# Performance work log

Measured on AMD Instinct MI355X. Metric: run time of the kernel, lower is better.

## Reference

```python
import jax, jax.numpy as jnp
import numpy as np

SEQ_LEN, BATCH, HID, INP = 512, 256, 256, 256


def setup_inputs() -> dict:
    key = jax.random.key(0)
    ks = jax.random.split(key, 6)
    s = 1.0 / np.sqrt(HID)  # torch GRUCell init scale
    return {
        "carry": jnp.zeros((BATCH, HID), jnp.float32),
        "seq_inputs": jax.random.normal(ks[0], (SEQ_LEN, BATCH, INP), jnp.float32),
        "seq_resets": jax.random.randint(ks[1], (SEQ_LEN, BATCH), 0, 2, jnp.int32),
        "w_ih": jax.random.uniform(ks[2], (3 * HID, INP), jnp.float32, -s, s),
        "w_hh": jax.random.uniform(ks[3], (3 * HID, HID), jnp.float32, -s, s),
        "b_ih": jax.random.uniform(ks[4], (3 * HID,), jnp.float32, -s, s),
        "b_hh": jax.random.uniform(ks[5], (3 * HID,), jnp.float32, -s, s),
    }


def reference(carry, seq_inputs, seq_resets, w_ih, w_hh, b_ih, b_hh):
    # Precompute the input-side projection for all timesteps in one GEMM.
    gi_all = jnp.einsum('tbi,gi->tbg', seq_inputs, w_ih) + b_ih  # (T,B,3H)

    def step(h, xs):
        gi, reset_t = xs
        h = jnp.where(reset_t[:, None] > 0, jnp.zeros_like(h), h)
        gh = h @ w_hh.T + b_hh  # (B,3H)
        i_r, i_z, i_n = jnp.split(gi, 3, axis=1)
        h_r, h_z, h_n = jnp.split(gh, 3, axis=1)
        r = jax.nn.sigmoid(i_r + h_r)
        z = jax.nn.sigmoid(i_z + h_z)
        n = jnp.tanh(i_n + r * h_n)
        h_new = (1.0 - z) * n + z * h
        return h_new, h_new

    h_final, outputs = jax.lax.scan(step, carry, (gi_all, seq_resets))
    return h_final, outputs
```

## Files before the change

### kernel.cpp

```cpp
#include <hip/hip_runtime.h>
#include <hip/hip_bf16.h>
#include <hip/hip_fp16.h>


#define T_LEN 512
#define BATCH 256
#define HID   256
#define G3    768

typedef __attribute__((ext_vector_type(8))) short s16x8;
typedef __attribute__((ext_vector_type(4))) float fx4;

#define MFMA16 __builtin_amdgcn_mfma_f32_16x16x32_bf16

__device__ __forceinline__ unsigned short f2bf(float f) {
  union { float f; unsigned u; } v; v.f = f;
  unsigned r = v.u + 0x7fffu + ((v.u >> 16) & 1u);
  return (unsigned short)(r >> 16);
}

__device__ __forceinline__ s16x8 pack8(float4 a, float4 b) {
  s16x8 f;
  f[0] = (short)f2bf(a.x); f[1] = (short)f2bf(a.y);
  f[2] = (short)f2bf(a.z); f[3] = (short)f2bf(a.w);
  f[4] = (short)f2bf(b.x); f[5] = (short)f2bf(b.y);
  f[6] = (short)f2bf(b.z); f[7] = (short)f2bf(b.w);
  return f;
}

__device__ __forceinline__ void load_weights(const float* __restrict__ W,
                                             s16x8 (&wr)[2][8], char* Wlds,
                                             int tid, int wid, int col, int kgrp) {
#pragma unroll
  for (int n = 0; n < 2; ++n) {
    int g = n * 256 + wid * 16 + col;
#pragma unroll
    for (int s8 = 0; s8 < 8; ++s8) {
      int k = s8 * 32 + kgrp * 8;
      const float4* p = (const float4*)(W + g * 256 + k);
      wr[n][s8] = pack8(p[0], p[1]);
    }
  }
#pragma unroll
  for (int q = 0; q < 8; ++q) {
    int li = tid + q * 1024;
    int wv = li >> 9, s8 = (li >> 6) & 7, l = li & 63;
    int g = 512 + wv * 16 + (l & 15);
    int k = s8 * 32 + (l >> 4) * 8;
    const float4* p = (const float4*)(W + g * 256 + k);
    *(s16x8*)(Wlds + li * 16) = pack8(p[0], p[1]);
  }
}

__global__ __launch_bounds__(1024) void gi_proj_kernel(
    const float* __restrict__ X, const float* __restrict__ w_ih,
    const float* __restrict__ b_ih, const float* __restrict__ b_hh,
    __half* __restrict__ gi) {
  __shared__ __align__(16) char Wlds[131072];
  __shared__ __align__(16) char Ald[8192];

  const int tid = threadIdx.x;
  const int wid = tid >> 6, lane = tid & 63;
  const int col = lane & 15, kgrp = lane >> 4;

  s16x8 wr[2][8];
  load_weights(w_ih, wr, Wlds, tid, wid, col, kgrp);

  float bias0, bias1, bias2;
  {
    int gb = wid * 16 + col;
    bias0 = b_ih[gb]       + b_hh[gb];
    bias1 = b_ih[256 + gb] + b_hh[256 + gb];
    bias2 = b_ih[512 + gb];
  }

  const int e4 = tid * 4;
  const int srow = e4 >> 8, sk = e4 & 255;
  const unsigned sbyte = ((unsigned)(srow * 512 + sk * 2)) ^ ((unsigned)(srow & 7) << 4);

  float4 xcur = *(const float4*)(X + (size_t)(blockIdx.x * 16 + srow) * 256 + sk);

  for (int chunk = blockIdx.x; chunk < (T_LEN * BATCH) / 16; chunk += 256) {
    __syncthreads();
    {
      unsigned lo = (unsigned)f2bf(xcur.x) | ((unsigned)f2bf(xcur.y) << 16);
      unsigned hi = (unsigned)f2bf(xcur.z) | ((unsigned)f2bf(xcur.w) << 16);
      uint2 v; v.x = lo; v.y = hi;
      *(uint2*)(Ald + sbyte) = v;
    }
    int nchunk = chunk + 256;
    if (nchunk < (T_LEN * BATCH) / 16)
      xcur = *(const float4*)(X + (size_t)(nchunk * 16 + srow) * 256 + sk);
    __syncthreads();

    fx4 acc0 = {0.f, 0.f, 0.f, 0.f}, acc1 = acc0, acc2 = acc0;
#pragma unroll
    for (int s8 = 0; s8 < 8; ++s8) {
      unsigned aoff = ((unsigned)(col * 512 + (s8 * 32 + kgrp * 8) * 2)) ^
                      ((unsigned)(col & 7) << 4);
      s16x8 af = *(const s16x8*)(Ald + aoff);
      s16x8 w2 = *(const s16x8*)(Wlds + ((wid * 8 + s8) * 64 + lane) * 16);
      acc0 = MFMA16(af, wr[0][s8], acc0, 0, 0, 0);
      acc1 = MFMA16(af, wr[1][s8], acc1, 0, 0, 0);
      acc2 = MFMA16(af, w2, acc2, 0, 0, 0);
    }

    size_t m0 = (size_t)chunk * 16;
#pragma unroll
    for (int j = 0; j < 4; ++j) {
      size_t m = m0 + kgrp * 4 + j;
      __half* gp = gi + m * G3 + wid * 16 + col;
      gp[0]   = __float2half(acc0[j] + bias0);
      gp[256] = __float2half(acc1[j] + bias1);
      gp[512] = __float2half(acc2[j] + bias2);
    }
  }
}

__global__ __launch_bounds__(1024) void gru_scan_kernel(
    const float* __restrict__ carry, const __half* __restrict__ gi,
    const int* __restrict__ resets, const float* __restrict__ w_hh,
    const float* __restrict__ b_hh, float* __restrict__ out) {
  __shared__ __align__(16) char Wlds[131072];
  __shared__ __align__(16) char Ald[8192];
  __shared__ int lastreset[16];

  const int tid = threadIdx.x;
  const int wid = tid >> 6, lane = tid & 63;
  const int col = lane & 15, kgrp = lane >> 4;
  const int c = blockIdx.x >> 4, bt = blockIdx.x & 15;
  const int b0 = bt * 16, t0 = c * 32, t1 = t0 + 32;
  const int hid = wid * 16 + col;

  s16x8 wr[2][8];
  load_weights(w_hh, wr, Wlds, tid, wid, col, kgrp);
  const float bhhn = b_hh[512 + hid];

  int s, useCarry;
  if (c == 0) {
    s = 0; useCarry = 1;
  } else {
    if (tid < 16) lastreset[tid] = -1;
    for (int base = t0 - 64;; base -= 64) {
      __syncthreads();
      int tt = base + (tid >> 4);
      if (tt >= 0 && tt < t0) {
        if (resets[tt * BATCH + b0 + (tid & 15)] != 0)
          atomicMax(&lastreset[tid & 15], tt);
      }
      __syncthreads();
      int mn = t0, all = 1;
#pragma unroll
      for (int i = 0; i < 16; ++i) {
        int v = lastreset[i];
        all &= (v >= 0) ? 1 : 0;
        mn = min(mn, v < 0 ? t0 : v);
      }
      if (all) { s = mn; useCarry = 0; break; }
      if (base <= 0) { s = 0; useCarry = 1; break; }
    }
  }

  {
    int e4 = tid * 4, row = e4 >> 8, k = e4 & 255;
    int rst = resets[s * BATCH + b0 + row];
    float4 v = {0.f, 0.f, 0.f, 0.f};
    if (useCarry && !rst) v = *(const float4*)(carry + (size_t)(b0 + row) * HID + k);
    unsigned lo = (unsigned)f2bf(v.x) | ((unsigned)f2bf(v.y) << 16);
    unsigned hi = (unsigned)f2bf(v.z) | ((unsigned)f2bf(v.w) << 16);
    unsigned byteoff = ((unsigned)(row * 512 + k * 2)) ^ ((unsigned)(row & 7) << 4);
    uint2 u; u.x = lo; u.y = hi;
    *(uint2*)(Ald + byteoff) = u;
  }
  float hprev[4];
#pragma unroll
  for (int j = 0; j < 4; ++j) {
    int b = kgrp * 4 + j;
    int rst = resets[s * BATCH + b0 + b];
    float hv = 0.f;
    if (useCarry && !rst) hv = carry[(size_t)(b0 + b) * HID + hid];
    hprev[j] = hv;
  }
  __syncthreads();

  for (int t = s; t < t1; ++t) {
    __half gr[4], gz[4], gn[4];
#pragma unroll
    for (int j = 0; j < 4; ++j) {
      const __half* gp = gi + ((size_t)t * BATCH + b0 + kgrp * 4 + j) * G3 + hid;
      gr[j] = gp[0]; gz[j] = gp[256]; gn[j] = gp[512];
    }
    int4 rn = {0, 0, 0, 0};
    if (t + 1 < T_LEN) rn = *(const int4*)(resets + (t + 1) * BATCH + b0 + kgrp * 4);

    fx4 acc0 = {0.f, 0.f, 0.f, 0.f}, acc1 = acc0, acc2 = acc0;
#pragma unroll
    for (int s8 = 0; s8 < 8; ++s8) {
      unsigned aoff = ((unsigned)(col * 512 + (s8 * 32 + kgrp * 8) * 2)) ^
                      ((unsigned)(col & 7) << 4);
      s16x8 af = *(const s16x8*)(Ald + aoff);
      s16x8 w2 = *(const s16x8*)(Wlds + ((wid * 8 + s8) * 64 + lane) * 16);
      acc0 = MFMA16(af, wr[0][s8], acc0, 0, 0, 0);
      acc1 = MFMA16(af, wr[1][s8], acc1, 0, 0, 0);
      acc2 = MFMA16(af, w2, acc2, 0, 0, 0);
    }
    __syncthreads();

    const bool wr_out = (t >= t0);
    float* op = out + 65536 + ((size_t)t * BATCH + b0) * HID;
#pragma unroll
    for (int j = 0; j < 4; ++j) {
      int b = kgrp * 4 + j;
      float pr = __half2float(gr[j]) + acc0[j];
      float pz = __half2float(gz[j]) + acc1[j];
      float r = __builtin_amdgcn_rcpf(1.f + __expf(-pr));
      float z = __builtin_amdgcn_rcpf(1.f + __expf(-pz));
      float pn = __half2float(gn[j]) + r * (acc2[j] + bhhn);
      float n = 1.f - 2.f * __builtin_amdgcn_rcpf(1.f + __expf(2.f * pn));
      float hnew = (1.f - z) * n + z * hprev[j];
      if (wr_out) op[(size_t)b * HID + hid] = hnew;
      int rj = (j == 0) ? rn.x : (j == 1) ? rn.y : (j == 2) ? rn.z : rn.w;
      float hk = rj ? 0.f : hnew;
      hprev[j] = hk;
      unsigned hoff = ((unsigned)(b * 512 + hid * 2)) ^ ((unsigned)(b & 7) << 4);
      *(unsigned short*)(Ald + hoff) = f2bf(hk);
    }
    __syncthreads();
  }

  if (c == 15) {
#pragma unroll
    for (int j = 0; j < 4; ++j)
      out[(size_t)(b0 + kgrp * 4 + j) * HID + hid] = hprev[j];
  }
}

extern "C" void kernel_launch(void* const* d_in, const int* in_sizes, int n_in,
                              void* d_out, int out_size, void* d_ws, size_t ws_size,
                              hipStream_t stream) {
  const float* carry = (const float*)d_in[0];
  const float* X     = (const float*)d_in[1];
  const int*   rsts  = (const int*)d_in[2];
  const float* w_ih  = (const float*)d_in[3];
  const float* w_hh  = (const float*)d_in[4];
  const float* b_ih  = (const float*)d_in[5];
  const float* b_hh  = (const float*)d_in[6];
  float* out = (float*)d_out;

  const size_t gi_bytes = (size_t)T_LEN * BATCH * G3 * sizeof(__half);
  if (ws_size < gi_bytes) return;
  __half* gi = (__half*)d_ws;

  gi_proj_kernel<<<256, 1024, 0, stream>>>(X, w_ih, b_ih, b_hh, gi);
  gru_scan_kernel<<<256, 1024, 0, stream>>>(carry, gi, rsts, w_hh, b_hh, out);
}
```

Before: 303.5 us.

## Double-buffer hidden state, prefetch gate inputs, transpose gi layout for vector loads

The hidden-state LDS tile is double-buffered so each timestep needs one barrier instead of two, and the barrier becomes a lighter custom s_barrier. The gi intermediate is stored gate-major and hidden-major with batch innermost, so each lane reads and writes four contiguous halves as one vector instead of scalar gathers. Next-step gate inputs and resets are prefetched a step ahead, and scan block IDs are remapped across batch tiles. This adds LDS and register pressure and relies on manual waitcnt and scheduling correctness.

```diff
diff --git a/kernel.cpp b/kernel.cpp
--- a/kernel.cpp
+++ b/kernel.cpp
@@ -6,12 +6,14 @@
 #define T_LEN 512
 #define BATCH 256
 #define HID   256
-#define G3    768
 
 typedef __attribute__((ext_vector_type(8))) short s16x8;
 typedef __attribute__((ext_vector_type(4))) float fx4;
+typedef __attribute__((ext_vector_type(4))) unsigned short u16x4;
 
 #define MFMA16 __builtin_amdgcn_mfma_f32_16x16x32_bf16
+#define GATE_STRIDE 65536u
+#define T_STRIDE    196608u
 
 __device__ __forceinline__ unsigned short f2bf(float f) {
   union { float f; unsigned u; } v; v.f = f;
@@ -52,12 +54,19 @@
   }
 }
 
+__device__ __forceinline__ void soft_barrier() {
+  asm volatile("s_waitcnt lgkmcnt(0)" ::: "memory");
+  __builtin_amdgcn_s_barrier();
+  __builtin_amdgcn_sched_barrier(0);
+  asm volatile("" ::: "memory");
+}
+
 __global__ __launch_bounds__(1024) void gi_proj_kernel(
     const float* __restrict__ X, const float* __restrict__ w_ih,
     const float* __restrict__ b_ih, const float* __restrict__ b_hh,
     __half* __restrict__ gi) {
   __shared__ __align__(16) char Wlds[131072];
-  __shared__ __align__(16) char Ald[8192];
+  __shared__ __align__(16) char Ald[2][8192];
 
   const int tid = threadIdx.x;
   const int wid = tid >> 6, lane = tid & 63;
@@ -80,40 +89,46 @@
 
   float4 xcur = *(const float4*)(X + (size_t)(blockIdx.x * 16 + srow) * 256 + sk);
 
+  int parity = 0;
   for (int chunk = blockIdx.x; chunk < (T_LEN * BATCH) / 16; chunk += 256) {
-    __syncthreads();
+    char* ab = Ald[parity];
     {
       unsigned lo = (unsigned)f2bf(xcur.x) | ((unsigned)f2bf(xcur.y) << 16);
       unsigned hi = (unsigned)f2bf(xcur.z) | ((unsigned)f2bf(xcur.w) << 16);
       uint2 v; v.x = lo; v.y = hi;
-      *(uint2*)(Ald + sbyte) = v;
+      *(uint2*)(ab + sbyte) = v;
     }
     int nchunk = chunk + 256;
     if (nchunk < (T_LEN * BATCH) / 16)
       xcur = *(const float4*)(X + (size_t)(nchunk * 16 + srow) * 256 + sk);
-    __syncthreads();
+
+    soft_barrier();
 
     fx4 acc0 = {0.f, 0.f, 0.f, 0.f}, acc1 = acc0, acc2 = acc0;
 #pragma unroll
     for (int s8 = 0; s8 < 8; ++s8) {
       unsigned aoff = ((unsigned)(col * 512 + (s8 * 32 + kgrp * 8) * 2)) ^
                       ((unsigned)(col & 7) << 4);
-      s16x8 af = *(const s16x8*)(Ald + aoff);
+      s16x8 af = *(const s16x8*)(ab + aoff);
       s16x8 w2 = *(const s16x8*)(Wlds + ((wid * 8 + s8) * 64 + lane) * 16);
       acc0 = MFMA16(af, wr[0][s8], acc0, 0, 0, 0);
       acc1 = MFMA16(af, wr[1][s8], acc1, 0, 0, 0);
       acc2 = MFMA16(af, w2, acc2, 0, 0, 0);
     }
 
-    size_t m0 = (size_t)chunk * 16;
+    int t = chunk >> 4, btile = chunk & 15;
+    __half* gb = gi + ((size_t)t * 3 * 256 + wid * 16 + col) * 256 + btile * 16 + kgrp * 4;
+    u16x4 o0, o1, o2;
 #pragma unroll
     for (int j = 0; j < 4; ++j) {
-      size_t m = m0 + kgrp * 4 + j;
-      __half* gp = gi + m * G3 + wid * 16 + col;
-      gp[0]   = __float2half(acc0[j] + bias0);
-      gp[256] = __float2half(acc1[j] + bias1);
-      gp[512] = __float2half(acc2[j] + bias2);
-    }
+      o0[j] = __half_as_ushort(__float2half(acc0[j] + bias0));
+      o1[j] = __half_as_ushort(__float2half(acc1[j] + bias1));
+      o2[j] = __half_as_ushort(__float2half(acc2[j] + bias2));
+    }
+    *(u16x4*)(gb) = o0;
+    *(u16x4*)(gb + GATE_STRIDE) = o1;
+    *(u16x4*)(gb + 2 * GATE_STRIDE) = o2;
+    parity ^= 1;
   }
 }
 
@@ -122,13 +137,15 @@
     const int* __restrict__ resets, const float* __restrict__ w_hh,
     const float* __restrict__ b_hh, float* __restrict__ out) {
   __shared__ __align__(16) char Wlds[131072];
-  __shared__ __align__(16) char Ald[8192];
+  __shared__ __align__(16) char Ald[2][8192];
   __shared__ int lastreset[16];
 
   const int tid = threadIdx.x;
   const int wid = tid >> 6, lane = tid & 63;
   const int col = lane & 15, kgrp = lane >> 4;
-  const int c = blockIdx.x >> 4, bt = blockIdx.x & 15;
+  const int bid = blockIdx.x;
+  const int bt = ((bid & 7) << 1) | ((bid >> 3) & 1);
+  const int c  = bid >> 4;
   const int b0 = bt * 16, t0 = c * 32, t1 = t0 + 32;
   const int hid = wid * 16 + col;
 
@@ -170,7 +187,7 @@
     unsigned hi = (unsigned)f2bf(v.z) | ((unsigned)f2bf(v.w) << 16);
     unsigned byteoff = ((unsigned)(row * 512 + k * 2)) ^ ((unsigned)(row & 7) << 4);
     uint2 u; u.x = lo; u.y = hi;
-    *(uint2*)(Ald + byteoff) = u;
+    *(uint2*)(Ald[0] + byteoff) = u;
   }
   float hprev[4];
 #pragma unroll
@@ -183,49 +200,62 @@
   }
   __syncthreads();
 
+  const __half* gp = gi + ((size_t)s * 3 * 256 + hid) * 256 + b0 + kgrp * 4;
+  float* op = out + 65536 + ((size_t)s * BATCH + b0 + kgrp * 4) * HID + hid;
+  const int* rbase = resets + b0 + kgrp * 4;
+
+  u16x4 gC0 = *(const u16x4*)(gp);
+  u16x4 gC1 = *(const u16x4*)(gp + GATE_STRIDE);
+  u16x4 gC2 = *(const u16x4*)(gp + 2 * GATE_STRIDE);
+  int4  rnC = *(const int4*)(rbase + (size_t)min(s + 1, T_LEN - 1) * BATCH);
+
   for (int t = s; t < t1; ++t) {
-    __half gr[4], gz[4], gn[4];
-#pragma unroll
-    for (int j = 0; j < 4; ++j) {
-      const __half* gp = gi + ((size_t)t * BATCH + b0 + kgrp * 4 + j) * G3 + hid;
-      gr[j] = gp[0]; gz[j] = gp[256]; gn[j] = gp[512];
-    }
-    int4 rn = {0, 0, 0, 0};
-    if (t + 1 < T_LEN) rn = *(const int4*)(resets + (t + 1) * BATCH + b0 + kgrp * 4);
-
+    const bool more = (t + 1 < t1);
+    const __half* gq = gp + (more ? T_STRIDE : 0u);
+    u16x4 gN0 = *(const u16x4*)(gq);
+    u16x4 gN1 = *(const u16x4*)(gq + GATE_STRIDE);
+    u16x4 gN2 = *(const u16x4*)(gq + 2 * GATE_STRIDE);
+    int4  rnN = *(const int4*)(rbase + (size_t)min(t + 2, T_LEN - 1) * BATCH);
+
+    const char* ab = Ald[(t - s) & 1];
     fx4 acc0 = {0.f, 0.f, 0.f, 0.f}, acc1 = acc0, acc2 = acc0;
 #pragma unroll
     for (int s8 = 0; s8 < 8; ++s8) {
       unsigned aoff = ((unsigned)(col * 512 + (s8 * 32 + kgrp * 8) * 2)) ^
                       ((unsigned)(col & 7) << 4);
-      s16x8 af = *(const s16x8*)(Ald + aoff);
+      s16x8 af = *(const s16x8*)(ab + aoff);
       s16x8 w2 = *(const s16x8*)(Wlds + ((wid * 8 + s8) * 64 + lane) * 16);
       acc0 = MFMA16(af, wr[0][s8], acc0, 0, 0, 0);
       acc1 = MFMA16(af, wr[1][s8], acc1, 0, 0, 0);
       acc2 = MFMA16(af, w2, acc2, 0, 0, 0);
     }
-    __syncthreads();
-
+
+    char* aw = (char*)Ald[((t - s) & 1) ^ 1];
     const bool wr_out = (t >= t0);
-    float* op = out + 65536 + ((size_t)t * BATCH + b0) * HID;
+    const bool lastT  = (t + 1 >= T_LEN);
 #pragma unroll
     for (int j = 0; j < 4; ++j) {
       int b = kgrp * 4 + j;
-      float pr = __half2float(gr[j]) + acc0[j];
-      float pz = __half2float(gz[j]) + acc1[j];
+      float pr = __half2float(__ushort_as_half(gC0[j])) + acc0[j];
+      float pz = __half2float(__ushort_as_half(gC1[j])) + acc1[j];
       float r = __builtin_amdgcn_rcpf(1.f + __expf(-pr));
       float z = __builtin_amdgcn_rcpf(1.f + __expf(-pz));
-      float pn = __half2float(gn[j]) + r * (acc2[j] + bhhn);
+      float pn = __half2float(__ushort_as_half(gC2[j])) + r * (acc2[j] + bhhn);
       float n = 1.f - 2.f * __builtin_amdgcn_rcpf(1.f + __expf(2.f * pn));
       float hnew = (1.f - z) * n + z * hprev[j];
-      if (wr_out) op[(size_t)b * HID + hid] = hnew;
-      int rj = (j == 0) ? rn.x : (j == 1) ? rn.y : (j == 2) ? rn.z : rn.w;
+      if (wr_out) op[j * HID] = hnew;
+      int rj = (j == 0) ? rnC.x : (j == 1) ? rnC.y : (j == 2) ? rnC.z : rnC.w;
+      if (lastT) rj = 0;
       float hk = rj ? 0.f : hnew;
       hprev[j] = hk;
       unsigned hoff = ((unsigned)(b * 512 + hid * 2)) ^ ((unsigned)(b & 7) << 4);
-      *(unsigned short*)(Ald + hoff) = f2bf(hk);
-    }
-    __syncthreads();
+      *(unsigned short*)(aw + hoff) = f2bf(hk);
+    }
+
+    gC0 = gN0; gC1 = gN1; gC2 = gN2; rnC = rnN;
+    gp = gq;
+    op += 65536;
+    soft_barrier();
   }
 
   if (c == 15) {
@@ -247,7 +277,7 @@
   const float* b_hh  = (const float*)d_in[6];
   float* out = (float*)d_out;
 
-  const size_t gi_bytes = (size_t)T_LEN * BATCH * G3 * sizeof(__half);
+  const size_t gi_bytes = (size_t)T_LEN * BATCH * 3 * HID * sizeof(__half);
   if (ws_size < gi_bytes) return;
   __half* gi = (__half*)d_ws;
 
```

Measured after the change: 397.8 us. +31.1%, slower.
